# Kernel optimization log

Hardware: AMD Instinct MI355X
Metric: run time of the kernel (lower is better)

## Reference

```python
import jax, jax.numpy as jnp
import numpy as np

EMBED_DIM = 1024
HEAD_SIZE = 64
B, T = 4, 4096


def setup_inputs() -> dict:
    key = jax.random.key(0)
    kx, kq, kk, kv = jax.random.split(key, 4)
    x = jax.random.normal(kx, (B, T, EMBED_DIM), dtype=jnp.float32)
    sw = 1.0 / np.sqrt(EMBED_DIM)  # kaiming-ish init scale for linear weights
    Wq = jax.random.normal(kq, (EMBED_DIM, HEAD_SIZE), dtype=jnp.float32) * sw
    Wk = jax.random.normal(kk, (EMBED_DIM, HEAD_SIZE), dtype=jnp.float32) * sw
    Wv = jax.random.normal(kv, (EMBED_DIM, HEAD_SIZE), dtype=jnp.float32) * sw
    return {"x": x, "Wq": Wq, "Wk": Wk, "Wv": Wv}


def reference(x, Wq, Wk, Wv):
    Bn, Tn, C = x.shape
    q = jnp.einsum('btc,ch->bth', x, Wq)
    k = jnp.einsum('btc,ch->bth', x, Wk)
    v = jnp.einsum('btc,ch->bth', x, Wv)
    # NOTE: original scales by sqrt(C) = sqrt(embed_dim), not sqrt(head_size)
    scale = 1.0 / jnp.sqrt(jnp.asarray(C, dtype=x.dtype))
    wei = jnp.einsum('bth,bsh->bts', q, k) * scale  # [B, T, T]
    causal = jnp.tril(jnp.ones((Tn, Tn), dtype=bool))
    wei = jnp.where(causal, wei, -jnp.inf)
    wei = jax.nn.softmax(wei, axis=-1)
    # dropout p=0.0 (eval mode): identity
    return jnp.einsum('bts,bsh->bth', wei, v)
```

## Files before the change

### kernel.cpp

```cpp
#include <hip/hip_runtime.h>
#include <cstdint>


typedef __bf16 bf16;
typedef __bf16 bf16x8 __attribute__((ext_vector_type(8)));
typedef float  f32x4  __attribute__((ext_vector_type(4)));

#define MFMA16(a, b, c) __builtin_amdgcn_mfma_f32_16x16x32_bf16((a), (b), (c), 0, 0, 0)

#if __has_builtin(__builtin_amdgcn_exp2f)
#define EXP2(x) __builtin_amdgcn_exp2f(x)
#else
#define EXP2(x) exp2f(x)
#endif

#define B_SZ 4
#define T_SZ 4096
#define C_SZ 1024
#define H_SZ 64
#define M_SZ (B_SZ * T_SZ)
#define QSCALE (1.4426950408889634f / 32.0f)
#define P_STR 8320

__device__ __forceinline__ void dma16(const void* g, void* l) {
    __builtin_amdgcn_global_load_lds(
        (const __attribute__((address_space(1))) uint32_t*)(uintptr_t)g,
        (__attribute__((address_space(3))) uint32_t*)(uint32_t)(uintptr_t)l,
        16, 0, 0);
}

__device__ __forceinline__ void pipe_sync() {
    asm volatile("s_waitcnt vmcnt(0)" ::: "memory");
    __builtin_amdgcn_s_barrier();
    __builtin_amdgcn_sched_barrier(0);
}

__global__ __launch_bounds__(256) void wt_prep(
    const float* __restrict__ Wq, const float* __restrict__ Wk,
    const float* __restrict__ Wv, bf16* __restrict__ wt2)
{
    const int n4 = blockIdx.x, t = threadIdx.x;
    const int nbase = n4 * 4;
    const float* W = (nbase < 64) ? Wq : (nbase < 128 ? Wk : Wv);
    const float sc = (nbase < 64) ? QSCALE : 1.0f;
    const int ncol = nbase & 63;
    #pragma unroll
    for (int i = 0; i < 4; ++i) {
        const int k = i * 256 + t;
        const float4 v = *(const float4*)(W + (size_t)k * H_SZ + ncol);
        const float vals[4] = {v.x, v.y, v.z, v.w};
        const size_t base = (size_t)(k >> 6) * 12288 + (size_t)((k >> 5) & 1) * 6144
                          + (size_t)((k >> 3) & 3) * 1536 + (k & 7);
        #pragma unroll
        for (int m = 0; m < 4; ++m)
            wt2[base + (size_t)(nbase + m) * 8] = (bf16)(vals[m] * sc);
    }
}

__global__ __launch_bounds__(256) void qkv_proj(
    const float* __restrict__ x, const bf16* __restrict__ wt2,
    bf16* __restrict__ qw, bf16* __restrict__ kw2, bf16* __restrict__ vtw2)
{
    const int m0 = blockIdx.x * 32;
    const int tid = threadIdx.x;
    const int wave = tid >> 6, lane = tid & 63;
    const int quad = lane >> 4, l15 = lane & 15;
    const int phase = blockIdx.x & 15;

    __shared__ __align__(16) float xs[2 * 4 * 32 * 8];
    __shared__ __align__(16) bf16  ws[2 * 4 * 192 * 8];

    f32x4 acc[2][3] = {};

    const char* xg = (const char*)x
        + (size_t)(m0 + ((tid >> 1) & 31)) * 4096
        + (size_t)((tid >> 6) & 3) * 32 + (size_t)(tid & 1) * 16;
    char* xl = (char*)xs + (size_t)tid * 16;
    const char* wg = (const char*)wt2 + (size_t)tid * 16;
    char* wl = (char*)ws + (size_t)tid * 16;

    for (int s = 0; s < 16; ++s) {
        const size_t se = (size_t)((s + phase) & 15);
        __syncthreads();
        dma16(xg + se * 256, xl);
        dma16(xg + se * 256 + 128, xl + 4096);
        #pragma unroll
        for (int i = 0; i < 6; ++i)
            dma16(wg + se * 24576 + (size_t)i * 4096, wl + (size_t)i * 4096);
        __syncthreads();

        #pragma unroll
        for (int ss = 0; ss < 2; ++ss) {
            bf16x8 a[2];
            #pragma unroll
            for (int mg = 0; mg < 2; ++mg) {
                const float* ap = xs + ss * 1024 + quad * 256 + (mg * 16 + l15) * 8;
                const f32x4 lo = *(const f32x4*)ap;
                const f32x4 hi = *(const f32x4*)(ap + 4);
                a[mg][0] = (bf16)lo[0]; a[mg][1] = (bf16)lo[1];
                a[mg][2] = (bf16)lo[2]; a[mg][3] = (bf16)lo[3];
                a[mg][4] = (bf16)hi[0]; a[mg][5] = (bf16)hi[1];
                a[mg][6] = (bf16)hi[2]; a[mg][7] = (bf16)hi[3];
            }
            #pragma unroll
            for (int i = 0; i < 3; ++i) {
                const int nt = wave * 3 + i;
                const bf16x8 wf = *(const bf16x8*)(ws + ss * 6144 + quad * 1536
                                                   + (nt * 16 + l15) * 8);
                #pragma unroll
                for (int mg = 0; mg < 2; ++mg)
                    acc[mg][i] = MFMA16(a[mg], wf, acc[mg][i]);
            }
        }
    }

    #pragma unroll
    for (int mg = 0; mg < 2; ++mg)
        #pragma unroll
        for (int i = 0; i < 3; ++i) {
            const int n = (wave * 3 + i) * 16 + l15;
            const int which = n >> 6, col = n & 63;
            #pragma unroll
            for (int r = 0; r < 4; ++r) {
                const int t = m0 + mg * 16 + quad * 4 + r;
                const bf16 v = (bf16)acc[mg][i][r];
                if (which == 0) {
                    qw[(size_t)t * H_SZ + col] = v;
                } else if (which == 1) {
                    kw2[(size_t)(t >> 6) * 4096
                        + (size_t)(((col >> 5) << 2) + ((col >> 3) & 3)) * 512
                        + (size_t)(t & 63) * 8 + (col & 7)] = v;
                } else {
                    vtw2[(size_t)(t >> 6) * 4096
                         + (size_t)((((t >> 5) & 1) << 2) + ((t >> 3) & 3)) * 512
                         + (size_t)col * 8 + (t & 7)] = v;
                }
            }
        }
}

__global__ __launch_bounds__(256) void flash_attn(
    const bf16* __restrict__ qw, const bf16* __restrict__ kw2,
    const bf16* __restrict__ vtw2, float* __restrict__ pbuf)
{
    const int bx = blockIdx.x;
    const int item = (bx & 1) ? (511 - (bx >> 1)) : (bx >> 1);
    const int qt2 = 31 - (item >> 4);
    const int b   = (item >> 2) & 3;
    const int h   = item & 3;
    const int i0  = qt2 * 128;
    const int nkv = qt2 * 2 + 2;

    const int tid = threadIdx.x;
    const int wave = tid >> 6, lane = tid & 63;
    const int quad = lane >> 4, l15 = lane & 15;

    __shared__ __align__(16) bf16 kvs[2][8192];
    __shared__ __align__(16) bf16 pls[4][32 * 72];

    bf16x8 aq[2][2];
    #pragma unroll
    for (int mg2 = 0; mg2 < 2; ++mg2) {
        const bf16* qp = qw + ((size_t)b * T_SZ + i0 + wave * 32 + mg2 * 16 + l15) * H_SZ
                       + quad * 8;
        aq[mg2][0] = *(const bf16x8*)qp;
        aq[mg2][1] = *(const bf16x8*)(qp + 32);
    }
    const bf16 onev = (bf16)1.0f;
    const bf16x8 vone = {onev, onev, onev, onev, onev, onev, onev, onev};

    const char* kgb = (const char*)kw2 + (size_t)b * 524288;
    const char* vgb = (const char*)vtw2 + (size_t)b * 524288;
    bf16* pl = pls[wave];

    f32x4 o[2][4] = {};
    f32x4 osum[2] = {};

    auto stage = [&](int jt, int buf) {
        const char* ks = kgb + (size_t)jt * 8192;
        const char* vs = vgb + (size_t)jt * 8192;
        char* dst = (char*)(&kvs[buf][0]) + (size_t)tid * 16;
        dma16(ks + (size_t)tid * 16, dst);
        dma16(ks + 4096 + (size_t)tid * 16, dst + 4096);
        dma16(vs + (size_t)tid * 16, dst + 8192);
        dma16(vs + 4096 + (size_t)tid * 16, dst + 12288);
    };

    if (h < nkv) {
        stage(h, 0);
        pipe_sync();
    }

    int c = 0;
    for (int jt = h; jt < nkv; jt += 4, c ^= 1) {
        if (jt + 4 < nkv) stage(jt + 4, c ^ 1);
        const bf16* kb = &kvs[c][0];
        const bf16* vb = &kvs[c][0] + 4096;

        f32x4 s4[2][4] = {};
        __builtin_amdgcn_s_setprio(1);
        #pragma unroll
        for (int ct = 0; ct < 4; ++ct) {
            const bf16x8 k0 = *(const bf16x8*)(kb + (0 * 4 + quad) * 512 + (ct * 16 + l15) * 8);
            const bf16x8 k1 = *(const bf16x8*)(kb + (1 * 4 + quad) * 512 + (ct * 16 + l15) * 8);
            #pragma unroll
            for (int mg2 = 0; mg2 < 2; ++mg2) {
                s4[mg2][ct] = MFMA16(aq[mg2][0], k0, s4[mg2][ct]);
                s4[mg2][ct] = MFMA16(aq[mg2][1], k1, s4[mg2][ct]);
            }
        }
        __builtin_amdgcn_s_setprio(0);

        if (jt >= 2 * qt2) {
            #pragma unroll
            for (int mg2 = 0; mg2 < 2; ++mg2) {
                const int grow = i0 + wave * 32 + mg2 * 16 + quad * 4;
                #pragma unroll
                for (int ct = 0; ct < 4; ++ct) {
                    const int gcol = jt * 64 + ct * 16 + l15;
                    #pragma unroll
                    for (int rr = 0; rr < 4; ++rr)
                        if (gcol > grow + rr) s4[mg2][ct][rr] = -3.0e38f;
                }
            }
        }

        #pragma unroll
        for (int mg2 = 0; mg2 < 2; ++mg2)
            #pragma unroll
            for (int ct = 0; ct < 4; ++ct)
                #pragma unroll
                for (int rr = 0; rr < 4; ++rr)
                    pl[(mg2 * 16 + quad * 4 + rr) * 72 + ct * 16 + l15]
                        = (bf16)EXP2(s4[mg2][ct][rr]);

        bf16x8 pa[2][2];
        #pragma unroll
        for (int mg2 = 0; mg2 < 2; ++mg2) {
            pa[mg2][0] = *(const bf16x8*)&pl[(mg2 * 16 + l15) * 72 + quad * 8];
            pa[mg2][1] = *(const bf16x8*)&pl[(mg2 * 16 + l15) * 72 + 32 + quad * 8];
        }

        __builtin_amdgcn_s_setprio(1);
        #pragma unroll
        for (int ht = 0; ht < 4; ++ht) {
            const bf16x8 v0 = *(const bf16x8*)(vb + (0 * 4 + quad) * 512 + (ht * 16 + l15) * 8);
            const bf16x8 v1 = *(const bf16x8*)(vb + (1 * 4 + quad) * 512 + (ht * 16 + l15) * 8);
            #pragma unroll
            for (int mg2 = 0; mg2 < 2; ++mg2) {
                o[mg2][ht] = MFMA16(pa[mg2][0], v0, o[mg2][ht]);
                o[mg2][ht] = MFMA16(pa[mg2][1], v1, o[mg2][ht]);
            }
        }
        #pragma unroll
        for (int mg2 = 0; mg2 < 2; ++mg2) {
            osum[mg2] = MFMA16(pa[mg2][0], vone, osum[mg2]);
            osum[mg2] = MFMA16(pa[mg2][1], vone, osum[mg2]);
        }
        __builtin_amdgcn_s_setprio(0);

        pipe_sync();
    }

    float* pb = pbuf + (size_t)(((b * 32 + qt2) * 4) + h) * P_STR;
    #pragma unroll
    for (int mg2 = 0; mg2 < 2; ++mg2) {
        const int L0 = wave * 32 + mg2 * 16 + quad * 4;
        #pragma unroll
        for (int ht = 0; ht < 4; ++ht)
            #pragma unroll
            for (int rr = 0; rr < 4; ++rr)
                pb[(L0 + rr) * 64 + ht * 16 + l15] = o[mg2][ht][rr];
        if (l15 == 0) {
            #pragma unroll
            for (int rr = 0; rr < 4; ++rr)
                pb[8192 + L0 + rr] = osum[mg2][rr];
        }
    }
}

__global__ __launch_bounds__(256) void combine(
    const float* __restrict__ pbuf, float* __restrict__ out)
{
    const int bq2 = blockIdx.x >> 1, tid = threadIdx.x;
    const int row = ((blockIdx.x & 1) << 6) + (tid >> 2);
    const int c0 = (tid & 3) * 16;
    const float* p = pbuf + (size_t)bq2 * 4 * P_STR;

    f32x4 a0 = {}, a1 = {}, a2 = {}, a3 = {};
    float l = 0.f;
    #pragma unroll
    for (int h = 0; h < 4; ++h) {
        const float* ph = p + (size_t)h * P_STR + row * 64 + c0;
        a0 += *(const f32x4*)(ph);
        a1 += *(const f32x4*)(ph + 4);
        a2 += *(const f32x4*)(ph + 8);
        a3 += *(const f32x4*)(ph + 12);
        l  += p[(size_t)h * P_STR + 8192 + row];
    }
    const float inv = 1.0f / l;
    float* op = out + ((size_t)bq2 * 128 + row) * 64 + c0;
    *(f32x4*)(op)      = a0 * inv;
    *(f32x4*)(op + 4)  = a1 * inv;
    *(f32x4*)(op + 8)  = a2 * inv;
    *(f32x4*)(op + 12) = a3 * inv;
}

extern "C" void kernel_launch(void* const* d_in, const int* in_sizes, int n_in,
                              void* d_out, int out_size, void* d_ws, size_t ws_size,
                              hipStream_t stream) {
    const float* x  = (const float*)d_in[0];
    const float* Wq = (const float*)d_in[1];
    const float* Wk = (const float*)d_in[2];
    const float* Wv = (const float*)d_in[3];

    bf16* qw   = (bf16*)d_ws;
    bf16* kw2  = qw + (size_t)M_SZ * H_SZ;
    bf16* vtw2 = kw2 + (size_t)M_SZ * H_SZ;
    bf16* wt2  = vtw2 + (size_t)M_SZ * H_SZ;
    float* pbuf = (float*)(wt2 + 3 * 64 * 1024);
    float* out = (float*)d_out;

    wt_prep<<<48, 256, 0, stream>>>(Wq, Wk, Wv, wt2);
    qkv_proj<<<M_SZ / 32, 256, 0, stream>>>(x, wt2, qw, kw2, vtw2);
    flash_attn<<<512, 256, 0, stream>>>(qw, kw2, vtw2, pbuf);
    combine<<<256, 256, 0, stream>>>(pbuf, out);
}
```

Measured before the change: 148.7 us.

## Pack P stores as bf16x4 with permuted V layout; store partials in bf16

```diff
diff --git a/kernel.cpp b/kernel.cpp
--- a/kernel.cpp
+++ b/kernel.cpp
@@ -3,6 +3,7 @@
 
 
 typedef __bf16 bf16;
+typedef __bf16 bf16x4 __attribute__((ext_vector_type(4)));
 typedef __bf16 bf16x8 __attribute__((ext_vector_type(8)));
 typedef float  f32x4  __attribute__((ext_vector_type(4)));
 
@@ -20,7 +21,8 @@
 #define H_SZ 64
 #define M_SZ (B_SZ * T_SZ)
 #define QSCALE (1.4426950408889634f / 32.0f)
-#define P_STR 8320
+#define P_O 8192
+#define P_L 128
 
 __device__ __forceinline__ void dma16(const void* g, void* l) {
     __builtin_amdgcn_global_load_lds(
@@ -131,9 +133,10 @@
                         + (size_t)(((col >> 5) << 2) + ((col >> 3) & 3)) * 512
                         + (size_t)(t & 63) * 8 + (col & 7)] = v;
                 } else {
+                    const int t6 = t & 63;
+                    const int p = ((t6 & 15) << 2) | (t6 >> 4);
                     vtw2[(size_t)(t >> 6) * 4096
-                         + (size_t)((((t >> 5) & 1) << 2) + ((t >> 3) & 3)) * 512
-                         + (size_t)col * 8 + (t & 7)] = v;
+                         + (size_t)(p >> 3) * 512 + (size_t)col * 8 + (p & 7)] = v;
                 }
             }
         }
@@ -141,7 +144,8 @@
 
 __global__ __launch_bounds__(256) void flash_attn(
     const bf16* __restrict__ qw, const bf16* __restrict__ kw2,
-    const bf16* __restrict__ vtw2, float* __restrict__ pbuf)
+    const bf16* __restrict__ vtw2, bf16* __restrict__ pbuf_o,
+    float* __restrict__ pbuf_l)
 {
     const int bx = blockIdx.x;
     const int item = (bx & 1) ? (511 - (bx >> 1)) : (bx >> 1);
@@ -228,11 +232,14 @@
         #pragma unroll
         for (int mg2 = 0; mg2 < 2; ++mg2)
             #pragma unroll
-            for (int ct = 0; ct < 4; ++ct)
-                #pragma unroll
-                for (int rr = 0; rr < 4; ++rr)
-                    pl[(mg2 * 16 + quad * 4 + rr) * 72 + ct * 16 + l15]
-                        = (bf16)EXP2(s4[mg2][ct][rr]);
+            for (int rr = 0; rr < 4; ++rr) {
+                bf16x4 pk;
+                pk[0] = (bf16)EXP2(s4[mg2][0][rr]);
+                pk[1] = (bf16)EXP2(s4[mg2][1][rr]);
+                pk[2] = (bf16)EXP2(s4[mg2][2][rr]);
+                pk[3] = (bf16)EXP2(s4[mg2][3][rr]);
+                *(bf16x4*)&pl[(mg2 * 16 + quad * 4 + rr) * 72 + l15 * 4] = pk;
+            }
 
         bf16x8 pa[2][2];
         #pragma unroll
@@ -262,7 +269,8 @@
         pipe_sync();
     }
 
-    float* pb = pbuf + (size_t)(((b * 32 + qt2) * 4) + h) * P_STR;
+    bf16* pb_o = pbuf_o + (size_t)(((b * 32 + qt2) * 4) + h) * P_O;
+    float* pb_l = pbuf_l + (size_t)(((b * 32 + qt2) * 4) + h) * P_L;
     #pragma unroll
     for (int mg2 = 0; mg2 < 2; ++mg2) {
         const int L0 = wave * 32 + mg2 * 16 + quad * 4;
@@ -270,40 +278,44 @@
         for (int ht = 0; ht < 4; ++ht)
             #pragma unroll
             for (int rr = 0; rr < 4; ++rr)
-                pb[(L0 + rr) * 64 + ht * 16 + l15] = o[mg2][ht][rr];
+                pb_o[(L0 + rr) * 64 + ht * 16 + l15] = (bf16)o[mg2][ht][rr];
         if (l15 == 0) {
             #pragma unroll
             for (int rr = 0; rr < 4; ++rr)
-                pb[8192 + L0 + rr] = osum[mg2][rr];
+                pb_l[L0 + rr] = osum[mg2][rr];
         }
     }
 }
 
 __global__ __launch_bounds__(256) void combine(
-    const float* __restrict__ pbuf, float* __restrict__ out)
+    const bf16* __restrict__ pbuf_o, const float* __restrict__ pbuf_l,
+    float* __restrict__ out)
 {
     const int bq2 = blockIdx.x >> 1, tid = threadIdx.x;
     const int row = ((blockIdx.x & 1) << 6) + (tid >> 2);
     const int c0 = (tid & 3) * 16;
-    const float* p = pbuf + (size_t)bq2 * 4 * P_STR;
-
-    f32x4 a0 = {}, a1 = {}, a2 = {}, a3 = {};
+
+    float a[16] = {};
     float l = 0.f;
     #pragma unroll
     for (int h = 0; h < 4; ++h) {
-        const float* ph = p + (size_t)h * P_STR + row * 64 + c0;
-        a0 += *(const f32x4*)(ph);
-        a1 += *(const f32x4*)(ph + 4);
-        a2 += *(const f32x4*)(ph + 8);
-        a3 += *(const f32x4*)(ph + 12);
-        l  += p[(size_t)h * P_STR + 8192 + row];
+        const bf16* ph = pbuf_o + (size_t)(bq2 * 4 + h) * P_O + row * 64 + c0;
+        const bf16x8 v0 = *(const bf16x8*)ph;
+        const bf16x8 v1 = *(const bf16x8*)(ph + 8);
+        #pragma unroll
+        for (int j = 0; j < 8; ++j) {
+            a[j]     += (float)v0[j];
+            a[8 + j] += (float)v1[j];
+        }
+        l += pbuf_l[(size_t)(bq2 * 4 + h) * P_L + row];
     }
     const float inv = 1.0f / l;
     float* op = out + ((size_t)bq2 * 128 + row) * 64 + c0;
-    *(f32x4*)(op)      = a0 * inv;
-    *(f32x4*)(op + 4)  = a1 * inv;
-    *(f32x4*)(op + 8)  = a2 * inv;
-    *(f32x4*)(op + 12) = a3 * inv;
+    #pragma unroll
+    for (int g = 0; g < 4; ++g) {
+        f32x4 v = {a[g * 4], a[g * 4 + 1], a[g * 4 + 2], a[g * 4 + 3]};
+        *(f32x4*)(op + g * 4) = v * inv;
+    }
 }
 
 extern "C" void kernel_launch(void* const* d_in, const int* in_sizes, int n_in,
@@ -318,11 +330,12 @@
     bf16* kw2  = qw + (size_t)M_SZ * H_SZ;
     bf16* vtw2 = kw2 + (size_t)M_SZ * H_SZ;
     bf16* wt2  = vtw2 + (size_t)M_SZ * H_SZ;
-    float* pbuf = (float*)(wt2 + 3 * 64 * 1024);
+    bf16* pbuf_o = wt2 + 3 * 64 * 1024;
+    float* pbuf_l = (float*)(pbuf_o + (size_t)512 * P_O);
     float* out = (float*)d_out;
 
     wt_prep<<<48, 256, 0, stream>>>(Wq, Wk, Wv, wt2);
     qkv_proj<<<M_SZ / 32, 256, 0, stream>>>(x, wt2, qw, kw2, vtw2);
-    flash_attn<<<512, 256, 0, stream>>>(qw, kw2, vtw2, pbuf);
-    combine<<<256, 256, 0, stream>>>(pbuf, out);
-}
+    flash_attn<<<512, 256, 0, stream>>>(qw, kw2, vtw2, pbuf_o, pbuf_l);
+    combine<<<256, 256, 0, stream>>>(pbuf_o, pbuf_l, out);
+}
```

Measured after the change: 143.8 us. -3.3%, faster.
